# Optimization experiments

Measured on AMD Instinct MI355X. Metric: run time of the kernel, lower is better.

## Reference

```python
import jax, jax.numpy as jnp
import numpy as np

D_MODEL = 1024
N_HEADS = 16
D_HEAD = D_MODEL // N_HEADS
SCALE = D_HEAD ** -0.5


def setup_inputs() -> dict:
    key = jax.random.key(0)
    ks = jax.random.split(key, 9)
    s = 0.02
    x = jax.random.normal(ks[0], (2, 2048, D_MODEL), dtype=jnp.float32)
    Wq = jax.random.normal(ks[1], (D_MODEL, D_MODEL), dtype=jnp.float32) * s
    Wk = jax.random.normal(ks[2], (D_MODEL, D_MODEL), dtype=jnp.float32) * s
    Wv = jax.random.normal(ks[3], (D_MODEL, D_MODEL), dtype=jnp.float32) * s
    Wo = jax.random.normal(ks[4], (D_MODEL, D_MODEL), dtype=jnp.float32) * s
    bq = jax.random.normal(ks[5], (D_MODEL,), dtype=jnp.float32) * s
    bk = jax.random.normal(ks[6], (D_MODEL,), dtype=jnp.float32) * s
    bv = jax.random.normal(ks[7], (D_MODEL,), dtype=jnp.float32) * s
    bo = jax.random.normal(ks[8], (D_MODEL,), dtype=jnp.float32) * s
    return {"x": x, "Wq": Wq, "bq": bq, "Wk": Wk, "bk": bk,
            "Wv": Wv, "bv": bv, "Wo": Wo, "bo": bo}


def reference(x, Wq, bq, Wk, bk, Wv, bv, Wo, bo):
    B, S, _ = x.shape
    # torch nn.Linear: y = x @ W.T + b
    def proj(W, b):
        h = jnp.einsum('bsd,ed->bse', x, W) + b
        return h.reshape(B, S, N_HEADS, D_HEAD).transpose(0, 2, 1, 3)  # [B,H,S,Dh]
    Q = proj(Wq, bq)
    K = proj(Wk, bk)
    V = proj(Wv, bv)
    # chunked QK^T softmax over full K == full attention (no mask, dropout=0)
    scores = jnp.einsum('bhqd,bhkd->bhqk', Q, K) * SCALE  # [B,H,S,S]
    attn = jax.nn.softmax(scores, axis=-1)
    out = jnp.einsum('bhqk,bhkd->bhqd', attn, V)
    out = out.transpose(0, 2, 1, 3).reshape(B, S, D_MODEL)
    return jnp.einsum('bsd,ed->bse', out, Wo) + bo
```

## Files before the change

kernel.cpp:

```cpp
#include <hip/hip_runtime.h>
#include <cstdint>
#include <cstddef>


typedef unsigned short u16;
typedef unsigned int u32;
typedef __bf16 bf16x8 __attribute__((ext_vector_type(8)));
typedef float f32x4 __attribute__((ext_vector_type(4)));

#define GLOAD_LDS16(gp, lp)                                                            \
  __builtin_amdgcn_global_load_lds((const __attribute__((address_space(1))) void*)(gp),\
                                   (__attribute__((address_space(3))) void*)(lp),      \
                                   16, 0, 0)

__device__ __forceinline__ u16 f2bf(float f) {
  unsigned u = __builtin_bit_cast(unsigned, f);
  u = u + 0x7fffu + ((u >> 16) & 1u);
  return (u16)(u >> 16);
}

__device__ __forceinline__ u32 cvtpk(float a, float b) {
  u32 r;
  asm("v_cvt_pk_bf16_f32 %0, %1, %2" : "=v"(r) : "v"(a), "v"(b));
  return r;
}

#define QSCALE 0.1803368801111204f

__global__ void cvt_all(const float* __restrict__ x,
                        const float* __restrict__ wq, const float* __restrict__ wk,
                        const float* __restrict__ wv, const float* __restrict__ wo,
                        u16* __restrict__ xb, u16* __restrict__ wqb,
                        u16* __restrict__ wkb, u16* __restrict__ wvb,
                        u16* __restrict__ wob) {
  int bx = blockIdx.x;
  const float* s; u16* d; int off;
  if (bx < 2048)      { s = x;  d = xb;  off = bx; }
  else if (bx < 2560) { s = wq; d = wqb; off = bx - 2048; }
  else if (bx < 3072) { s = wk; d = wkb; off = bx - 2560; }
  else if (bx < 3584) { s = wv; d = wvb; off = bx - 3072; }
  else                { s = wo; d = wob; off = bx - 3584; }
  int i = off * 2048 + threadIdx.x * 8;
  float4 a = *(const float4*)(s + i);
  float4 b = *(const float4*)(s + i + 4);
  uint4 o;
  o.x = f2bf(a.x) | ((u32)f2bf(a.y) << 16);
  o.y = f2bf(a.z) | ((u32)f2bf(a.w) << 16);
  o.z = f2bf(b.x) | ((u32)f2bf(b.y) << 16);
  o.w = f2bf(b.z) | ((u32)f2bf(b.w) << 16);
  *(uint4*)(d + i) = o;
}

template <int MODE, int BM, int BN>
__global__ __launch_bounds__(256, MODE == 0 ? 3 : 4) void gemm_mfma(
    const u16* __restrict__ A,
    const u16* __restrict__ W0, const u16* __restrict__ W1, const u16* __restrict__ W2,
    const float* __restrict__ b0, const float* __restrict__ b1, const float* __restrict__ b2,
    u16* __restrict__ o0, u16* __restrict__ o1, u16* __restrict__ o2,
    float* __restrict__ oF)
{
  constexpr int MF = BM / 32;
  constexpr int NF = BN / 32;
  constexpr int AG = BM / 32;
  constexpr int BG = BN / 32;
  constexpr int KU = (MODE == 0) ? 1 : 2;

  __shared__ __align__(16) u16 As[KU][BM * 64];
  __shared__ __align__(16) u16 Bs[KU][BN * 64];

  const int tid = threadIdx.x;
  const int w = tid >> 6, l = tid & 63;
  const int lane = l & 15, quad = l >> 4;
  const int wm = w >> 1, wn = w & 1;

  const int idb = blockIdx.y * gridDim.x + blockIdx.x;
  const int xcd = idb & 7, j = idb >> 3;
  int m_idx, n_idx;
  if (MODE == 0) {
    m_idx = (xcd >> 1) * 8 + (j & 7);
    n_idx = (xcd & 1) * 12 + (j >> 3);
  } else {
    m_idx = (xcd >> 1) * 16 + (j & 15);
    n_idx = (xcd & 1) * 8 + (j >> 4);
  }
  const int m0 = m_idx * BM;
  const int n0g = n_idx * BN;

  const int src = (MODE == 0) ? (n0g >> 10) : 0;
  const u16* Wsel = (MODE == 0) ? (src == 0 ? W0 : (src == 1 ? W1 : W2)) : W0;
  const float* bsel = (MODE == 0) ? (src == 0 ? b0 : (src == 1 ? b1 : b2)) : b0;
  const int n_base = (MODE == 0) ? (n0g & 1023) : n0g;

  const int c8 = ((l & 7) ^ (l >> 3)) * 8;
  const int lrow = l >> 3;

  f32x4 acc[MF][NF] = {};

  for (int kt = 0; kt < 1024; kt += 64 * KU) {
    __syncthreads();
    #pragma unroll
    for (int ku = 0; ku < KU; ++ku) {
      const u16* Ag = A + (size_t)m0 * 1024 + kt + ku * 64;
      const u16* Bg = Wsel + (size_t)n_base * 1024 + kt + ku * 64;
      #pragma unroll
      for (int i = 0; i < AG; ++i) {
        int rr = w * (8 * AG) + i * 8;
        GLOAD_LDS16(Ag + (size_t)(rr + lrow) * 1024 + c8, As[ku] + rr * 64);
      }
      #pragma unroll
      for (int i = 0; i < BG; ++i) {
        int rr = w * (8 * BG) + i * 8;
        GLOAD_LDS16(Bg + (size_t)(rr + lrow) * 1024 + c8, Bs[ku] + rr * 64);
      }
    }
    __syncthreads();

    #pragma unroll
    for (int ku = 0; ku < KU; ++ku) {
      bf16x8 af[MF][2], bf[NF][2];
      #pragma unroll
      for (int mf = 0; mf < MF; ++mf)
        #pragma unroll
        for (int ks = 0; ks < 2; ++ks)
          af[mf][ks] = *(const bf16x8*)((const char*)As[ku] +
              (wm * (BM / 2) + mf * 16 + lane) * 128 + (((ks * 4 + quad) ^ (lane & 7)) * 16));
      #pragma unroll
      for (int nf = 0; nf < NF; ++nf)
        #pragma unroll
        for (int ks = 0; ks < 2; ++ks)
          bf[nf][ks] = *(const bf16x8*)((const char*)Bs[ku] +
              (wn * (BN / 2) + nf * 16 + lane) * 128 + (((ks * 4 + quad) ^ (lane & 7)) * 16));
      #pragma unroll
      for (int ks = 0; ks < 2; ++ks)
        #pragma unroll
        for (int mf = 0; mf < MF; ++mf)
          #pragma unroll
          for (int nf = 0; nf < NF; ++nf)
            acc[mf][nf] = __builtin_amdgcn_mfma_f32_16x16x32_bf16(
                af[mf][ks], bf[nf][ks], acc[mf][nf], 0, 0, 0);
    }
  }

  float bb[NF];
  #pragma unroll
  for (int nf = 0; nf < NF; ++nf)
    bb[nf] = bsel[n_base + wn * (BN / 2) + nf * 16 + lane];

  u16* osel = (MODE == 0) ? (src == 0 ? o0 : (src == 1 ? o1 : o2)) : o0;

  #pragma unroll
  for (int mf = 0; mf < MF; ++mf) {
    int mb = m0 + wm * (BM / 2) + mf * 16 + quad * 4;
    #pragma unroll
    for (int nf = 0; nf < NF; ++nf) {
      int n_l = wn * (BN / 2) + nf * 16 + lane;
      if (MODE == 0 && src != 1) {
        float sc = (src == 0) ? QSCALE : 1.0f;
        float v0 = (acc[mf][nf][0] + bb[nf]) * sc;
        float v1 = (acc[mf][nf][1] + bb[nf]) * sc;
        float v2 = (acc[mf][nf][2] + bb[nf]) * sc;
        float v3 = (acc[mf][nf][3] + bb[nf]) * sc;
        int bi = mb >> 11, s = mb & 2047;
        int n_in = n_base + n_l;
        int h = n_in >> 6, dh = n_in & 63;
        uint2 pk = make_uint2(cvtpk(v0, v1), cvtpk(v2, v3));
        *(uint2*)(osel + (((size_t)(bi * 16 + h) * 64 + dh) * 2048 + s)) = pk;
      } else {
        #pragma unroll
        for (int r = 0; r < 4; ++r) {
          float v = acc[mf][nf][r] + bb[nf];
          int m = mb + r;
          if (MODE == 0) {
            int bi = m >> 11, s = m & 2047;
            int n_in = n_base + n_l;
            int h = n_in >> 6, dh = n_in & 63;
            osel[(((size_t)(bi * 16 + h) * 2048 + s) << 6) + dh] = f2bf(v);
          } else {
            oF[(size_t)m * 1024 + n0g + n_l] = v;
          }
        }
      }
    }
  }
}

union SMemU {
  struct {
    u16 K[2][64 * 64];
    u16 V[2][64 * 64];
  } m;
  struct {
    float O[2][32 * 64];
    float L[2][32];
  } f;
};

__global__ __launch_bounds__(256, 4) void attn_mfma(
    const u16* __restrict__ Qg_, const u16* __restrict__ Kg_,
    const u16* __restrict__ VTg_, u16* __restrict__ Og)
{
  __shared__ __align__(16) SMemU sm;

  const int tid = threadIdx.x;
  const int w = tid >> 6, l = tid & 63;
  const int lane = l & 15, quad = l >> 4;
  const int g = w >> 1;
  const int kh = w & 1;

  const int idb = blockIdx.y * gridDim.x + blockIdx.x;
  const int lid = (idb & 7) * 128 + (idb >> 3);
  const int bh = lid >> 5;
  const int q0 = (lid & 31) * 64;

  const u16* QTg = Qg_ + (size_t)bh * 64 * 2048;
  const u16* Kg  = Kg_ + (size_t)bh * 2048 * 64;
  const u16* VTg = VTg_ + (size_t)bh * 64 * 2048;

  const int c8 = ((l & 7) ^ (l >> 3)) * 8;
  const int lrow = l >> 3;
  const int rr = w * 16;

  const int qcol = q0 + g * 32 + lane;
  bf16x8 bq[2][2];
  #pragma unroll
  for (int qf = 0; qf < 2; ++qf)
    #pragma unroll
    for (int ks = 0; ks < 2; ++ks) {
      bf16x8 v;
      #pragma unroll
      for (int j = 0; j < 8; ++j)
        v[j] = __builtin_bit_cast(__bf16,
            QTg[(size_t)(ks * 32 + quad * 8 + j) * 2048 + qcol + qf * 16]);
      bq[qf][ks] = v;
    }

  GLOAD_LDS16(Kg + (size_t)(rr + lrow) * 64 + c8, sm.m.K[0] + rr * 64);
  GLOAD_LDS16(Kg + (size_t)(rr + 8 + lrow) * 64 + c8, sm.m.K[0] + (rr + 8) * 64);
  GLOAD_LDS16(VTg + (size_t)(rr + lrow) * 2048 + c8, sm.m.V[0] + rr * 64);
  GLOAD_LDS16(VTg + (size_t)(rr + 8 + lrow) * 2048 + c8, sm.m.V[0] + (rr + 8) * 64);

  f32x4 oa[2][4] = {};
  float lsum[2] = {0.f, 0.f};

  for (int kt = 0; kt < 32; ++kt) {
    const int cur = kt & 1;
    asm volatile("s_waitcnt vmcnt(0)" ::: "memory");
    __builtin_amdgcn_s_barrier();
    asm volatile("" ::: "memory");

    if (kt < 31) {
      GLOAD_LDS16(Kg + (size_t)((kt + 1) * 64 + rr + lrow) * 64 + c8,
                  sm.m.K[cur ^ 1] + rr * 64);
      GLOAD_LDS16(Kg + (size_t)((kt + 1) * 64 + rr + 8 + lrow) * 64 + c8,
                  sm.m.K[cur ^ 1] + (rr + 8) * 64);
      GLOAD_LDS16(VTg + (size_t)(rr + lrow) * 2048 + (kt + 1) * 64 + c8,
                  sm.m.V[cur ^ 1] + rr * 64);
      GLOAD_LDS16(VTg + (size_t)(rr + 8 + lrow) * 2048 + (kt + 1) * 64 + c8,
                  sm.m.V[cur ^ 1] + (rr + 8) * 64);
    }

    f32x4 sa[2][2] = {};
    #pragma unroll
    for (int ks = 0; ks < 2; ++ks) {
      bf16x8 ak[2];
      #pragma unroll
      for (int kf = 0; kf < 2; ++kf)
        ak[kf] = *(const bf16x8*)((const char*)sm.m.K[cur] +
            (kh * 32 + kf * 16 + lane) * 128 + (((ks * 4 + quad) ^ (lane & 7)) * 16));
      #pragma unroll
      for (int kf = 0; kf < 2; ++kf)
        #pragma unroll
        for (int qf = 0; qf < 2; ++qf)
          sa[kf][qf] = __builtin_amdgcn_mfma_f32_16x16x32_bf16(
              ak[kf], bq[qf][ks], sa[kf][qf], 0, 0, 0);
    }

    bf16x8 ap[2];
    #pragma unroll
    for (int qf = 0; qf < 2; ++qf) {
      float x0 = __builtin_amdgcn_exp2f(sa[0][qf][0]);
      float x1 = __builtin_amdgcn_exp2f(sa[0][qf][1]);
      float x2 = __builtin_amdgcn_exp2f(sa[0][qf][2]);
      float x3 = __builtin_amdgcn_exp2f(sa[0][qf][3]);
      float y0 = __builtin_amdgcn_exp2f(sa[1][qf][0]);
      float y1 = __builtin_amdgcn_exp2f(sa[1][qf][1]);
      float y2 = __builtin_amdgcn_exp2f(sa[1][qf][2]);
      float y3 = __builtin_amdgcn_exp2f(sa[1][qf][3]);
      lsum[qf] += ((x0 + x1) + (x2 + x3)) + ((y0 + y1) + (y2 + y3));
      u32 X0 = cvtpk(x0, x1), X1 = cvtpk(x2, x3);
      u32 Y0 = cvtpk(y0, y1), Y1 = cvtpk(y2, y3);
      asm("v_permlane32_swap_b32 %0, %1" : "+v"(X0), "+v"(Y0));
      asm("v_permlane16_swap_b32 %0, %1" : "+v"(X0), "+v"(Y0));
      asm("v_permlane32_swap_b32 %0, %1" : "+v"(X1), "+v"(Y1));
      asm("v_permlane16_swap_b32 %0, %1" : "+v"(X1), "+v"(Y1));
      uint4 d4 = make_uint4(X0, X1, Y0, Y1);
      ap[qf] = __builtin_bit_cast(bf16x8, d4);
    }

    {
      bf16x8 bv[4];
      #pragma unroll
      for (int df = 0; df < 4; ++df)
        bv[df] = *(const bf16x8*)((const char*)sm.m.V[cur] +
            (df * 16 + lane) * 128 + (((kh * 4 + quad) ^ (lane & 7)) * 16));
      #pragma unroll
      for (int qf = 0; qf < 2; ++qf)
        #pragma unroll
        for (int df = 0; df < 4; ++df)
          oa[qf][df] = __builtin_amdgcn_mfma_f32_16x16x32_bf16(
              ap[qf], bv[df], oa[qf][df], 0, 0, 0);
    }
  }

  #pragma unroll
  for (int qf = 0; qf < 2; ++qf) {
    lsum[qf] += __shfl_xor(lsum[qf], 16);
    lsum[qf] += __shfl_xor(lsum[qf], 32);
  }

  __syncthreads();
  if (kh == 1) {
    #pragma unroll
    for (int qf = 0; qf < 2; ++qf)
      #pragma unroll
      for (int df = 0; df < 4; ++df)
        #pragma unroll
        for (int r = 0; r < 4; ++r)
          sm.f.O[g][(qf * 16 + quad * 4 + r) * 64 + df * 16 + lane] = oa[qf][df][r];
    if (l < 16) {
      sm.f.L[g][l] = lsum[0];
      sm.f.L[g][16 + l] = lsum[1];
    }
  }
  __syncthreads();
  if (kh == 0) {
    const int b = bh >> 4, hh = bh & 15;
    u16* Ob = Og + ((size_t)b * 2048 + q0 + g * 32) * 1024 + hh * 64;
    float ltot[2];
    #pragma unroll
    for (int qf = 0; qf < 2; ++qf)
      ltot[qf] = lsum[qf] + sm.f.L[g][qf * 16 + lane];
    #pragma unroll
    for (int qf = 0; qf < 2; ++qf)
      #pragma unroll
      for (int r = 0; r < 4; ++r) {
        float inv = 1.0f / __shfl(ltot[qf], quad * 4 + r, 16);
        int qrow = qf * 16 + quad * 4 + r;
        #pragma unroll
        for (int df = 0; df < 4; ++df) {
          float v = oa[qf][df][r] + sm.f.O[g][qrow * 64 + df * 16 + lane];
          Ob[(size_t)qrow * 1024 + df * 16 + lane] = f2bf(v * inv);
        }
      }
  }
}

extern "C" void kernel_launch(void* const* d_in, const int* in_sizes, int n_in,
                              void* d_out, int out_size, void* d_ws, size_t ws_size,
                              hipStream_t stream)
{
  (void)in_sizes; (void)n_in; (void)out_size; (void)ws_size;
  const float* x  = (const float*)d_in[0];
  const float* Wq = (const float*)d_in[1];
  const float* bq = (const float*)d_in[2];
  const float* Wk = (const float*)d_in[3];
  const float* bk = (const float*)d_in[4];
  const float* Wv = (const float*)d_in[5];
  const float* bv = (const float*)d_in[6];
  const float* Wo = (const float*)d_in[7];
  const float* bo = (const float*)d_in[8];
  float* y = (float*)d_out;

  const size_t NM = (size_t)4096 * 1024;
  u16* xb  = (u16*)d_ws;
  u16* wqb = xb + NM;
  u16* wkb = wqb + 1024 * 1024;
  u16* wvb = wkb + 1024 * 1024;
  u16* wob = wvb + 1024 * 1024;
  u16* Qb  = wob + 1024 * 1024;
  u16* Kb  = Qb + NM;
  u16* VTb = Kb + NM;
  u16* AOb = VTb + NM;

  cvt_all<<<4096, 256, 0, stream>>>(x, Wq, Wk, Wv, Wo, xb, wqb, wkb, wvb, wob);

  gemm_mfma<0, 128, 128><<<dim3(24, 32), 256, 0, stream>>>(
      xb, wqb, wkb, wvb, bq, bk, bv, Qb, Kb, VTb, nullptr);

  attn_mfma<<<dim3(32, 32), 256, 0, stream>>>(Qb, Kb, VTb, AOb);

  gemm_mfma<1, 64, 64><<<dim3(16, 64), 256, 0, stream>>>(
      AOb, wob, nullptr, nullptr, bo, nullptr, nullptr,
      nullptr, nullptr, nullptr, y);
}
```

Measured before the change: 178.7 us.

## Fuse all four kernels into one persistent kernel with grid-wide barriers

```diff
diff --git a/kernel.cpp b/kernel.cpp
--- a/kernel.cpp
+++ b/kernel.cpp
@@ -27,331 +27,361 @@
 
 #define QSCALE 0.1803368801111204f
 
-__global__ void cvt_all(const float* __restrict__ x,
-                        const float* __restrict__ wq, const float* __restrict__ wk,
-                        const float* __restrict__ wv, const float* __restrict__ wo,
-                        u16* __restrict__ xb, u16* __restrict__ wqb,
-                        u16* __restrict__ wkb, u16* __restrict__ wvb,
-                        u16* __restrict__ wob) {
-  int bx = blockIdx.x;
-  const float* s; u16* d; int off;
-  if (bx < 2048)      { s = x;  d = xb;  off = bx; }
-  else if (bx < 2560) { s = wq; d = wqb; off = bx - 2048; }
-  else if (bx < 3072) { s = wk; d = wkb; off = bx - 2560; }
-  else if (bx < 3584) { s = wv; d = wvb; off = bx - 3072; }
-  else                { s = wo; d = wob; off = bx - 3584; }
-  int i = off * 2048 + threadIdx.x * 8;
-  float4 a = *(const float4*)(s + i);
-  float4 b = *(const float4*)(s + i + 4);
-  uint4 o;
-  o.x = f2bf(a.x) | ((u32)f2bf(a.y) << 16);
-  o.y = f2bf(a.z) | ((u32)f2bf(a.w) << 16);
-  o.z = f2bf(b.x) | ((u32)f2bf(b.y) << 16);
-  o.w = f2bf(b.z) | ((u32)f2bf(b.w) << 16);
-  *(uint4*)(d + i) = o;
+union MegaSmem {
+  struct { u16 As[128 * 64]; u16 Bs[128 * 64]; } g0;
+  struct { u16 As[2][64 * 64]; u16 Bs[2][64 * 64]; } g1;
+  struct { u16 K[2][64 * 64]; u16 V[2][64 * 64]; } am;
+  struct { float O[2][32 * 64]; float L[2][32]; } af;
+};
+
+__device__ __forceinline__ void gbar(u32* c, u32 nblk) {
+  __syncthreads();
+  if (threadIdx.x == 0) {
+    __threadfence();
+    __hip_atomic_fetch_add(c, 1u, __ATOMIC_ACQ_REL, __HIP_MEMORY_SCOPE_AGENT);
+    while (__hip_atomic_load(c, __ATOMIC_RELAXED, __HIP_MEMORY_SCOPE_AGENT) < nblk)
+      __builtin_amdgcn_s_sleep(2);
+    __threadfence();
+  }
+  __syncthreads();
 }
 
-template <int MODE, int BM, int BN>
-__global__ __launch_bounds__(256, MODE == 0 ? 3 : 4) void gemm_mfma(
-    const u16* __restrict__ A,
-    const u16* __restrict__ W0, const u16* __restrict__ W1, const u16* __restrict__ W2,
-    const float* __restrict__ b0, const float* __restrict__ b1, const float* __restrict__ b2,
-    u16* __restrict__ o0, u16* __restrict__ o1, u16* __restrict__ o2,
-    float* __restrict__ oF)
+__global__ __launch_bounds__(256, 4) void mega(
+    const float* __restrict__ x,
+    const float* __restrict__ Wq, const float* __restrict__ bq,
+    const float* __restrict__ Wk, const float* __restrict__ bk,
+    const float* __restrict__ Wv, const float* __restrict__ bv,
+    const float* __restrict__ Wo, const float* __restrict__ bo,
+    u16* __restrict__ xb, u16* __restrict__ wqb, u16* __restrict__ wkb,
+    u16* __restrict__ wvb, u16* __restrict__ wob,
+    u16* __restrict__ Qb, u16* __restrict__ Kb, u16* __restrict__ VTb,
+    u16* __restrict__ AOb, float* __restrict__ y, u32* __restrict__ ctr)
 {
-  constexpr int MF = BM / 32;
-  constexpr int NF = BN / 32;
-  constexpr int AG = BM / 32;
-  constexpr int BG = BN / 32;
-  constexpr int KU = (MODE == 0) ? 1 : 2;
-
-  __shared__ __align__(16) u16 As[KU][BM * 64];
-  __shared__ __align__(16) u16 Bs[KU][BN * 64];
+  __shared__ __align__(16) MegaSmem sm;
 
   const int tid = threadIdx.x;
+  const int idb = blockIdx.x;
   const int w = tid >> 6, l = tid & 63;
   const int lane = l & 15, quad = l >> 4;
-  const int wm = w >> 1, wn = w & 1;
-
-  const int idb = blockIdx.y * gridDim.x + blockIdx.x;
-  const int xcd = idb & 7, j = idb >> 3;
-  int m_idx, n_idx;
-  if (MODE == 0) {
-    m_idx = (xcd >> 1) * 8 + (j & 7);
-    n_idx = (xcd & 1) * 12 + (j >> 3);
-  } else {
-    m_idx = (xcd >> 1) * 16 + (j & 15);
-    n_idx = (xcd & 1) * 8 + (j >> 4);
-  }
-  const int m0 = m_idx * BM;
-  const int n0g = n_idx * BN;
-
-  const int src = (MODE == 0) ? (n0g >> 10) : 0;
-  const u16* Wsel = (MODE == 0) ? (src == 0 ? W0 : (src == 1 ? W1 : W2)) : W0;
-  const float* bsel = (MODE == 0) ? (src == 0 ? b0 : (src == 1 ? b1 : b2)) : b0;
-  const int n_base = (MODE == 0) ? (n0g & 1023) : n0g;
-
   const int c8 = ((l & 7) ^ (l >> 3)) * 8;
   const int lrow = l >> 3;
 
-  f32x4 acc[MF][NF] = {};
-
-  for (int kt = 0; kt < 1024; kt += 64 * KU) {
-    __syncthreads();
-    #pragma unroll
-    for (int ku = 0; ku < KU; ++ku) {
-      const u16* Ag = A + (size_t)m0 * 1024 + kt + ku * 64;
-      const u16* Bg = Wsel + (size_t)n_base * 1024 + kt + ku * 64;
-      #pragma unroll
-      for (int i = 0; i < AG; ++i) {
-        int rr = w * (8 * AG) + i * 8;
-        GLOAD_LDS16(Ag + (size_t)(rr + lrow) * 1024 + c8, As[ku] + rr * 64);
-      }
-      #pragma unroll
-      for (int i = 0; i < BG; ++i) {
-        int rr = w * (8 * BG) + i * 8;
-        GLOAD_LDS16(Bg + (size_t)(rr + lrow) * 1024 + c8, Bs[ku] + rr * 64);
-      }
-    }
-    __syncthreads();
-
-    #pragma unroll
-    for (int ku = 0; ku < KU; ++ku) {
-      bf16x8 af[MF][2], bf[NF][2];
-      #pragma unroll
-      for (int mf = 0; mf < MF; ++mf)
-        #pragma unroll
-        for (int ks = 0; ks < 2; ++ks)
-          af[mf][ks] = *(const bf16x8*)((const char*)As[ku] +
-              (wm * (BM / 2) + mf * 16 + lane) * 128 + (((ks * 4 + quad) ^ (lane & 7)) * 16));
-      #pragma unroll
-      for (int nf = 0; nf < NF; ++nf)
-        #pragma unroll
-        for (int ks = 0; ks < 2; ++ks)
-          bf[nf][ks] = *(const bf16x8*)((const char*)Bs[ku] +
-              (wn * (BN / 2) + nf * 16 + lane) * 128 + (((ks * 4 + quad) ^ (lane & 7)) * 16));
-      #pragma unroll
-      for (int ks = 0; ks < 2; ++ks)
-        #pragma unroll
-        for (int mf = 0; mf < MF; ++mf)
-          #pragma unroll
-          for (int nf = 0; nf < NF; ++nf)
+  for (int u = idb; u < 4096; u += 1024) {
+    const float* s; u16* d; int off;
+    if (u < 2048)      { s = x;  d = xb;  off = u; }
+    else if (u < 2560) { s = Wq; d = wqb; off = u - 2048; }
+    else if (u < 3072) { s = Wk; d = wkb; off = u - 2560; }
+    else if (u < 3584) { s = Wv; d = wvb; off = u - 3072; }
+    else               { s = Wo; d = wob; off = u - 3584; }
+    int i = off * 2048 + tid * 8;
+    float4 a = *(const float4*)(s + i);
+    float4 b = *(const float4*)(s + i + 4);
+    uint4 o;
+    o.x = f2bf(a.x) | ((u32)f2bf(a.y) << 16);
+    o.y = f2bf(a.z) | ((u32)f2bf(a.w) << 16);
+    o.z = f2bf(b.x) | ((u32)f2bf(b.y) << 16);
+    o.w = f2bf(b.z) | ((u32)f2bf(b.w) << 16);
+    *(uint4*)(d + i) = o;
+  }
+  gbar(ctr + 0, 1024);
+
+  if (idb < 768) {
+    const int xcd = idb & 7, j = idb >> 3;
+    const int m_idx = (xcd >> 1) * 8 + (j & 7);
+    const int n_idx = (xcd & 1) * 12 + (j >> 3);
+    const int m0 = m_idx * 128;
+    const int n0g = n_idx * 128;
+    const int src = n0g >> 10;
+    const u16* Wsel = (src == 0) ? wqb : (src == 1 ? wkb : wvb);
+    const float* bsel = (src == 0) ? bq : (src == 1 ? bk : bv);
+    const int n_base = n0g & 1023;
+    const int wm = w >> 1, wn = w & 1;
+
+    f32x4 acc[4][4] = {};
+
+    for (int kt = 0; kt < 1024; kt += 64) {
+      __syncthreads();
+      const u16* Ag = xb + (size_t)m0 * 1024 + kt;
+      const u16* Bg = Wsel + (size_t)n_base * 1024 + kt;
+      #pragma unroll
+      for (int i = 0; i < 4; ++i) {
+        int rr = w * 32 + i * 8;
+        GLOAD_LDS16(Ag + (size_t)(rr + lrow) * 1024 + c8, sm.g0.As + rr * 64);
+        GLOAD_LDS16(Bg + (size_t)(rr + lrow) * 1024 + c8, sm.g0.Bs + rr * 64);
+      }
+      __syncthreads();
+
+      #pragma unroll
+      for (int ks = 0; ks < 2; ++ks) {
+        bf16x8 af[4], bf[4];
+        #pragma unroll
+        for (int mf = 0; mf < 4; ++mf)
+          af[mf] = *(const bf16x8*)((const char*)sm.g0.As +
+              (wm * 64 + mf * 16 + lane) * 128 + (((ks * 4 + quad) ^ (lane & 7)) * 16));
+        #pragma unroll
+        for (int nf = 0; nf < 4; ++nf)
+          bf[nf] = *(const bf16x8*)((const char*)sm.g0.Bs +
+              (wn * 64 + nf * 16 + lane) * 128 + (((ks * 4 + quad) ^ (lane & 7)) * 16));
+        #pragma unroll
+        for (int mf = 0; mf < 4; ++mf)
+          #pragma unroll
+          for (int nf = 0; nf < 4; ++nf)
             acc[mf][nf] = __builtin_amdgcn_mfma_f32_16x16x32_bf16(
-                af[mf][ks], bf[nf][ks], acc[mf][nf], 0, 0, 0);
-    }
-  }
-
-  float bb[NF];
-  #pragma unroll
-  for (int nf = 0; nf < NF; ++nf)
-    bb[nf] = bsel[n_base + wn * (BN / 2) + nf * 16 + lane];
-
-  u16* osel = (MODE == 0) ? (src == 0 ? o0 : (src == 1 ? o1 : o2)) : o0;
-
-  #pragma unroll
-  for (int mf = 0; mf < MF; ++mf) {
-    int mb = m0 + wm * (BM / 2) + mf * 16 + quad * 4;
-    #pragma unroll
-    for (int nf = 0; nf < NF; ++nf) {
-      int n_l = wn * (BN / 2) + nf * 16 + lane;
-      if (MODE == 0 && src != 1) {
-        float sc = (src == 0) ? QSCALE : 1.0f;
-        float v0 = (acc[mf][nf][0] + bb[nf]) * sc;
-        float v1 = (acc[mf][nf][1] + bb[nf]) * sc;
-        float v2 = (acc[mf][nf][2] + bb[nf]) * sc;
-        float v3 = (acc[mf][nf][3] + bb[nf]) * sc;
-        int bi = mb >> 11, s = mb & 2047;
-        int n_in = n_base + n_l;
-        int h = n_in >> 6, dh = n_in & 63;
-        uint2 pk = make_uint2(cvtpk(v0, v1), cvtpk(v2, v3));
-        *(uint2*)(osel + (((size_t)(bi * 16 + h) * 64 + dh) * 2048 + s)) = pk;
-      } else {
-        #pragma unroll
-        for (int r = 0; r < 4; ++r) {
-          float v = acc[mf][nf][r] + bb[nf];
-          int m = mb + r;
-          if (MODE == 0) {
+                af[mf], bf[nf], acc[mf][nf], 0, 0, 0);
+      }
+    }
+
+    float bb[4];
+    #pragma unroll
+    for (int nf = 0; nf < 4; ++nf) bb[nf] = bsel[n_base + wn * 64 + nf * 16 + lane];
+
+    u16* osel = (src == 0) ? Qb : (src == 1 ? Kb : VTb);
+
+    #pragma unroll
+    for (int mf = 0; mf < 4; ++mf) {
+      int mb = m0 + wm * 64 + mf * 16 + quad * 4;
+      #pragma unroll
+      for (int nf = 0; nf < 4; ++nf) {
+        int n_l = wn * 64 + nf * 16 + lane;
+        if (src != 1) {
+          float sc = (src == 0) ? QSCALE : 1.0f;
+          float v0 = (acc[mf][nf][0] + bb[nf]) * sc;
+          float v1 = (acc[mf][nf][1] + bb[nf]) * sc;
+          float v2 = (acc[mf][nf][2] + bb[nf]) * sc;
+          float v3 = (acc[mf][nf][3] + bb[nf]) * sc;
+          int bi = mb >> 11, s = mb & 2047;
+          int n_in = n_base + n_l;
+          int h = n_in >> 6, dh = n_in & 63;
+          uint2 pk = make_uint2(cvtpk(v0, v1), cvtpk(v2, v3));
+          *(uint2*)(osel + (((size_t)(bi * 16 + h) * 64 + dh) * 2048 + s)) = pk;
+        } else {
+          #pragma unroll
+          for (int r = 0; r < 4; ++r) {
+            float v = acc[mf][nf][r] + bb[nf];
+            int m = mb + r;
             int bi = m >> 11, s = m & 2047;
             int n_in = n_base + n_l;
             int h = n_in >> 6, dh = n_in & 63;
             osel[(((size_t)(bi * 16 + h) * 2048 + s) << 6) + dh] = f2bf(v);
-          } else {
-            oF[(size_t)m * 1024 + n0g + n_l] = v;
           }
         }
       }
     }
   }
-}
-
-union SMemU {
-  struct {
-    u16 K[2][64 * 64];
-    u16 V[2][64 * 64];
-  } m;
-  struct {
-    float O[2][32 * 64];
-    float L[2][32];
-  } f;
-};
-
-__global__ __launch_bounds__(256, 4) void attn_mfma(
-    const u16* __restrict__ Qg_, const u16* __restrict__ Kg_,
-    const u16* __restrict__ VTg_, u16* __restrict__ Og)
-{
-  __shared__ __align__(16) SMemU sm;
-
-  const int tid = threadIdx.x;
-  const int w = tid >> 6, l = tid & 63;
-  const int lane = l & 15, quad = l >> 4;
-  const int g = w >> 1;
-  const int kh = w & 1;
-
-  const int idb = blockIdx.y * gridDim.x + blockIdx.x;
-  const int lid = (idb & 7) * 128 + (idb >> 3);
-  const int bh = lid >> 5;
-  const int q0 = (lid & 31) * 64;
-
-  const u16* QTg = Qg_ + (size_t)bh * 64 * 2048;
-  const u16* Kg  = Kg_ + (size_t)bh * 2048 * 64;
-  const u16* VTg = VTg_ + (size_t)bh * 64 * 2048;
-
-  const int c8 = ((l & 7) ^ (l >> 3)) * 8;
-  const int lrow = l >> 3;
-  const int rr = w * 16;
-
-  const int qcol = q0 + g * 32 + lane;
-  bf16x8 bq[2][2];
-  #pragma unroll
-  for (int qf = 0; qf < 2; ++qf)
-    #pragma unroll
-    for (int ks = 0; ks < 2; ++ks) {
-      bf16x8 v;
-      #pragma unroll
-      for (int j = 0; j < 8; ++j)
-        v[j] = __builtin_bit_cast(__bf16,
-            QTg[(size_t)(ks * 32 + quad * 8 + j) * 2048 + qcol + qf * 16]);
-      bq[qf][ks] = v;
-    }
-
-  GLOAD_LDS16(Kg + (size_t)(rr + lrow) * 64 + c8, sm.m.K[0] + rr * 64);
-  GLOAD_LDS16(Kg + (size_t)(rr + 8 + lrow) * 64 + c8, sm.m.K[0] + (rr + 8) * 64);
-  GLOAD_LDS16(VTg + (size_t)(rr + lrow) * 2048 + c8, sm.m.V[0] + rr * 64);
-  GLOAD_LDS16(VTg + (size_t)(rr + 8 + lrow) * 2048 + c8, sm.m.V[0] + (rr + 8) * 64);
-
-  f32x4 oa[2][4] = {};
-  float lsum[2] = {0.f, 0.f};
-
-  for (int kt = 0; kt < 32; ++kt) {
-    const int cur = kt & 1;
-    asm volatile("s_waitcnt vmcnt(0)" ::: "memory");
-    __builtin_amdgcn_s_barrier();
-    asm volatile("" ::: "memory");
-
-    if (kt < 31) {
-      GLOAD_LDS16(Kg + (size_t)((kt + 1) * 64 + rr + lrow) * 64 + c8,
-                  sm.m.K[cur ^ 1] + rr * 64);
-      GLOAD_LDS16(Kg + (size_t)((kt + 1) * 64 + rr + 8 + lrow) * 64 + c8,
-                  sm.m.K[cur ^ 1] + (rr + 8) * 64);
-      GLOAD_LDS16(VTg + (size_t)(rr + lrow) * 2048 + (kt + 1) * 64 + c8,
-                  sm.m.V[cur ^ 1] + rr * 64);
-      GLOAD_LDS16(VTg + (size_t)(rr + 8 + lrow) * 2048 + (kt + 1) * 64 + c8,
-                  sm.m.V[cur ^ 1] + (rr + 8) * 64);
-    }
-
-    f32x4 sa[2][2] = {};
-    #pragma unroll
-    for (int ks = 0; ks < 2; ++ks) {
-      bf16x8 ak[2];
-      #pragma unroll
-      for (int kf = 0; kf < 2; ++kf)
-        ak[kf] = *(const bf16x8*)((const char*)sm.m.K[cur] +
-            (kh * 32 + kf * 16 + lane) * 128 + (((ks * 4 + quad) ^ (lane & 7)) * 16));
-      #pragma unroll
-      for (int kf = 0; kf < 2; ++kf)
+  gbar(ctr + 1, 1024);
+
+  {
+    const int g = w >> 1;
+    const int kh = w & 1;
+    const int lid = (idb & 7) * 128 + (idb >> 3);
+    const int bh = lid >> 5;
+    const int q0 = (lid & 31) * 64;
+
+    const u16* QTg = Qb + (size_t)bh * 64 * 2048;
+    const u16* Kg  = Kb + (size_t)bh * 2048 * 64;
+    const u16* VTg = VTb + (size_t)bh * 64 * 2048;
+
+    const int rr = w * 16;
+
+    const int qcol = q0 + g * 32 + lane;
+    bf16x8 bq_[2][2];
+    #pragma unroll
+    for (int qf = 0; qf < 2; ++qf)
+      #pragma unroll
+      for (int ks = 0; ks < 2; ++ks) {
+        bf16x8 v;
+        #pragma unroll
+        for (int jj = 0; jj < 8; ++jj)
+          v[jj] = __builtin_bit_cast(__bf16,
+              QTg[(size_t)(ks * 32 + quad * 8 + jj) * 2048 + qcol + qf * 16]);
+        bq_[qf][ks] = v;
+      }
+
+    GLOAD_LDS16(Kg + (size_t)(rr + lrow) * 64 + c8, sm.am.K[0] + rr * 64);
+    GLOAD_LDS16(Kg + (size_t)(rr + 8 + lrow) * 64 + c8, sm.am.K[0] + (rr + 8) * 64);
+    GLOAD_LDS16(VTg + (size_t)(rr + lrow) * 2048 + c8, sm.am.V[0] + rr * 64);
+    GLOAD_LDS16(VTg + (size_t)(rr + 8 + lrow) * 2048 + c8, sm.am.V[0] + (rr + 8) * 64);
+
+    f32x4 oa[2][4] = {};
+    float lsum[2] = {0.f, 0.f};
+
+    for (int kt = 0; kt < 32; ++kt) {
+      const int cur = kt & 1;
+      asm volatile("s_waitcnt vmcnt(0)" ::: "memory");
+      __builtin_amdgcn_s_barrier();
+      asm volatile("" ::: "memory");
+
+      if (kt < 31) {
+        GLOAD_LDS16(Kg + (size_t)((kt + 1) * 64 + rr + lrow) * 64 + c8,
+                    sm.am.K[cur ^ 1] + rr * 64);
+        GLOAD_LDS16(Kg + (size_t)((kt + 1) * 64 + rr + 8 + lrow) * 64 + c8,
+                    sm.am.K[cur ^ 1] + (rr + 8) * 64);
+        GLOAD_LDS16(VTg + (size_t)(rr + lrow) * 2048 + (kt + 1) * 64 + c8,
+                    sm.am.V[cur ^ 1] + rr * 64);
+        GLOAD_LDS16(VTg + (size_t)(rr + 8 + lrow) * 2048 + (kt + 1) * 64 + c8,
+                    sm.am.V[cur ^ 1] + (rr + 8) * 64);
+      }
+
+      f32x4 sa[2][2] = {};
+      #pragma unroll
+      for (int ks = 0; ks < 2; ++ks) {
+        bf16x8 ak[2];
+        #pragma unroll
+        for (int kf = 0; kf < 2; ++kf)
+          ak[kf] = *(const bf16x8*)((const char*)sm.am.K[cur] +
+              (kh * 32 + kf * 16 + lane) * 128 + (((ks * 4 + quad) ^ (lane & 7)) * 16));
+        #pragma unroll
+        for (int kf = 0; kf < 2; ++kf)
+          #pragma unroll
+          for (int qf = 0; qf < 2; ++qf)
+            sa[kf][qf] = __builtin_amdgcn_mfma_f32_16x16x32_bf16(
+                ak[kf], bq_[qf][ks], sa[kf][qf], 0, 0, 0);
+      }
+
+      bf16x8 ap[2];
+      #pragma unroll
+      for (int qf = 0; qf < 2; ++qf) {
+        float x0 = __builtin_amdgcn_exp2f(sa[0][qf][0]);
+        float x1 = __builtin_amdgcn_exp2f(sa[0][qf][1]);
+        float x2 = __builtin_amdgcn_exp2f(sa[0][qf][2]);
+        float x3 = __builtin_amdgcn_exp2f(sa[0][qf][3]);
+        float y0 = __builtin_amdgcn_exp2f(sa[1][qf][0]);
+        float y1 = __builtin_amdgcn_exp2f(sa[1][qf][1]);
+        float y2 = __builtin_amdgcn_exp2f(sa[1][qf][2]);
+        float y3 = __builtin_amdgcn_exp2f(sa[1][qf][3]);
+        lsum[qf] += ((x0 + x1) + (x2 + x3)) + ((y0 + y1) + (y2 + y3));
+        u32 X0 = cvtpk(x0, x1), X1 = cvtpk(x2, x3);
+        u32 Y0 = cvtpk(y0, y1), Y1 = cvtpk(y2, y3);
+        asm("v_permlane32_swap_b32 %0, %1" : "+v"(X0), "+v"(Y0));
+        asm("v_permlane16_swap_b32 %0, %1" : "+v"(X0), "+v"(Y0));
+        asm("v_permlane32_swap_b32 %0, %1" : "+v"(X1), "+v"(Y1));
+        asm("v_permlane16_swap_b32 %0, %1" : "+v"(X1), "+v"(Y1));
+        uint4 d4 = make_uint4(X0, X1, Y0, Y1);
+        ap[qf] = __builtin_bit_cast(bf16x8, d4);
+      }
+
+      {
+        bf16x8 bv_[4];
+        #pragma unroll
+        for (int df = 0; df < 4; ++df)
+          bv_[df] = *(const bf16x8*)((const char*)sm.am.V[cur] +
+              (df * 16 + lane) * 128 + (((kh * 4 + quad) ^ (lane & 7)) * 16));
         #pragma unroll
         for (int qf = 0; qf < 2; ++qf)
-          sa[kf][qf] = __builtin_amdgcn_mfma_f32_16x16x32_bf16(
-              ak[kf], bq[qf][ks], sa[kf][qf], 0, 0, 0);
-    }
-
-    bf16x8 ap[2];
+          #pragma unroll
+          for (int df = 0; df < 4; ++df)
+            oa[qf][df] = __builtin_amdgcn_mfma_f32_16x16x32_bf16(
+                ap[qf], bv_[df], oa[qf][df], 0, 0, 0);
+      }
+    }
+
     #pragma unroll
     for (int qf = 0; qf < 2; ++qf) {
-      float x0 = __builtin_amdgcn_exp2f(sa[0][qf][0]);
-      float x1 = __builtin_amdgcn_exp2f(sa[0][qf][1]);
-      float x2 = __builtin_amdgcn_exp2f(sa[0][qf][2]);
-      float x3 = __builtin_amdgcn_exp2f(sa[0][qf][3]);
-      float y0 = __builtin_amdgcn_exp2f(sa[1][qf][0]);
-      float y1 = __builtin_amdgcn_exp2f(sa[1][qf][1]);
-      float y2 = __builtin_amdgcn_exp2f(sa[1][qf][2]);
-      float y3 = __builtin_amdgcn_exp2f(sa[1][qf][3]);
-      lsum[qf] += ((x0 + x1) + (x2 + x3)) + ((y0 + y1) + (y2 + y3));
-      u32 X0 = cvtpk(x0, x1), X1 = cvtpk(x2, x3);
-      u32 Y0 = cvtpk(y0, y1), Y1 = cvtpk(y2, y3);
-      asm("v_permlane32_swap_b32 %0, %1" : "+v"(X0), "+v"(Y0));
-      asm("v_permlane16_swap_b32 %0, %1" : "+v"(X0), "+v"(Y0));
-      asm("v_permlane32_swap_b32 %0, %1" : "+v"(X1), "+v"(Y1));
-      asm("v_permlane16_swap_b32 %0, %1" : "+v"(X1), "+v"(Y1));
-      uint4 d4 = make_uint4(X0, X1, Y0, Y1);
-      ap[qf] = __builtin_bit_cast(bf16x8, d4);
-    }
-
-    {
-      bf16x8 bv[4];
-      #pragma unroll
-      for (int df = 0; df < 4; ++df)
-        bv[df] = *(const bf16x8*)((const char*)sm.m.V[cur] +
-            (df * 16 + lane) * 128 + (((kh * 4 + quad) ^ (lane & 7)) * 16));
+      lsum[qf] += __shfl_xor(lsum[qf], 16);
+      lsum[qf] += __shfl_xor(lsum[qf], 32);
+    }
+
+    __syncthreads();
+    if (kh == 1) {
       #pragma unroll
       for (int qf = 0; qf < 2; ++qf)
         #pragma unroll
         for (int df = 0; df < 4; ++df)
-          oa[qf][df] = __builtin_amdgcn_mfma_f32_16x16x32_bf16(
-              ap[qf], bv[df], oa[qf][df], 0, 0, 0);
+          #pragma unroll
+          for (int r = 0; r < 4; ++r)
+            sm.af.O[g][(qf * 16 + quad * 4 + r) * 64 + df * 16 + lane] = oa[qf][df][r];
+      if (l < 16) {
+        sm.af.L[g][l] = lsum[0];
+        sm.af.L[g][16 + l] = lsum[1];
+      }
+    }
+    __syncthreads();
+    if (kh == 0) {
+      const int b = bh >> 4, hh = bh & 15;
+      u16* Ob = AOb + ((size_t)b * 2048 + q0 + g * 32) * 1024 + hh * 64;
+      float ltot[2];
+      #pragma unroll
+      for (int qf = 0; qf < 2; ++qf)
+        ltot[qf] = lsum[qf] + sm.af.L[g][qf * 16 + lane];
+      #pragma unroll
+      for (int qf = 0; qf < 2; ++qf)
+        #pragma unroll
+        for (int r = 0; r < 4; ++r) {
+          float inv = 1.0f / __shfl(ltot[qf], quad * 4 + r, 16);
+          int qrow = qf * 16 + quad * 4 + r;
+          #pragma unroll
+          for (int df = 0; df < 4; ++df) {
+            float v = oa[qf][df][r] + sm.af.O[g][qrow * 64 + df * 16 + lane];
+            Ob[(size_t)qrow * 1024 + df * 16 + lane] = f2bf(v * inv);
+          }
+        }
     }
   }
-
-  #pragma unroll
-  for (int qf = 0; qf < 2; ++qf) {
-    lsum[qf] += __shfl_xor(lsum[qf], 16);
-    lsum[qf] += __shfl_xor(lsum[qf], 32);
-  }
-
-  __syncthreads();
-  if (kh == 1) {
-    #pragma unroll
-    for (int qf = 0; qf < 2; ++qf)
-      #pragma unroll
-      for (int df = 0; df < 4; ++df)
+  gbar(ctr + 2, 1024);
+
+  {
+    const int xcd = idb & 7, j = idb >> 3;
+    const int m_idx = (xcd >> 1) * 16 + (j & 15);
+    const int n_idx = (xcd & 1) * 8 + (j >> 4);
+    const int m0 = m_idx * 64;
+    const int n0g = n_idx * 64;
+    const int wm = w >> 1, wn = w & 1;
+
+    f32x4 acc[2][2] = {};
+
+    for (int kt = 0; kt < 1024; kt += 128) {
+      __syncthreads();
+      #pragma unroll
+      for (int ku = 0; ku < 2; ++ku) {
+        const u16* Ag = AOb + (size_t)m0 * 1024 + kt + ku * 64;
+        const u16* Bg = wob + (size_t)n0g * 1024 + kt + ku * 64;
+        {
+          int rr = w * 16;
+          GLOAD_LDS16(Ag + (size_t)(rr + lrow) * 1024 + c8, sm.g1.As[ku] + rr * 64);
+          GLOAD_LDS16(Ag + (size_t)(rr + 8 + lrow) * 1024 + c8, sm.g1.As[ku] + (rr + 8) * 64);
+          GLOAD_LDS16(Bg + (size_t)(rr + lrow) * 1024 + c8, sm.g1.Bs[ku] + rr * 64);
+          GLOAD_LDS16(Bg + (size_t)(rr + 8 + lrow) * 1024 + c8, sm.g1.Bs[ku] + (rr + 8) * 64);
+        }
+      }
+      __syncthreads();
+
+      #pragma unroll
+      for (int ku = 0; ku < 2; ++ku)
+        #pragma unroll
+        for (int ks = 0; ks < 2; ++ks) {
+          bf16x8 af[2], bf[2];
+          #pragma unroll
+          for (int mf = 0; mf < 2; ++mf)
+            af[mf] = *(const bf16x8*)((const char*)sm.g1.As[ku] +
+                (wm * 32 + mf * 16 + lane) * 128 + (((ks * 4 + quad) ^ (lane & 7)) * 16));
+          #pragma unroll
+          for (int nf = 0; nf < 2; ++nf)
+            bf[nf] = *(const bf16x8*)((const char*)sm.g1.Bs[ku] +
+                (wn * 32 + nf * 16 + lane) * 128 + (((ks * 4 + quad) ^ (lane & 7)) * 16));
+          #pragma unroll
+          for (int mf = 0; mf < 2; ++mf)
+            #pragma unroll
+            for (int nf = 0; nf < 2; ++nf)
+              acc[mf][nf] = __builtin_amdgcn_mfma_f32_16x16x32_bf16(
+                  af[mf], bf[nf], acc[mf][nf], 0, 0, 0);
+        }
+    }
+
+    float bb[2];
+    #pragma unroll
+    for (int nf = 0; nf < 2; ++nf) bb[nf] = bo[n0g + wn * 32 + nf * 16 + lane];
+
+    #pragma unroll
+    for (int mf = 0; mf < 2; ++mf) {
+      int mb = m0 + wm * 32 + mf * 16 + quad * 4;
+      #pragma unroll
+      for (int nf = 0; nf < 2; ++nf) {
+        int n_l = wn * 32 + nf * 16 + lane;
         #pragma unroll
         for (int r = 0; r < 4; ++r)
-          sm.f.O[g][(qf * 16 + quad * 4 + r) * 64 + df * 16 + lane] = oa[qf][df][r];
-    if (l < 16) {
-      sm.f.L[g][l] = lsum[0];
-      sm.f.L[g][16 + l] = lsum[1];
-    }
-  }
-  __syncthreads();
-  if (kh == 0) {
-    const int b = bh >> 4, hh = bh & 15;
-    u16* Ob = Og + ((size_t)b * 2048 + q0 + g * 32) * 1024 + hh * 64;
-    float ltot[2];
-    #pragma unroll
-    for (int qf = 0; qf < 2; ++qf)
-      ltot[qf] = lsum[qf] + sm.f.L[g][qf * 16 + lane];
-    #pragma unroll
-    for (int qf = 0; qf < 2; ++qf)
-      #pragma unroll
-      for (int r = 0; r < 4; ++r) {
-        float inv = 1.0f / __shfl(ltot[qf], quad * 4 + r, 16);
-        int qrow = qf * 16 + quad * 4 + r;
-        #pragma unroll
-        for (int df = 0; df < 4; ++df) {
-          float v = oa[qf][df][r] + sm.f.O[g][qrow * 64 + df * 16 + lane];
-          Ob[(size_t)qrow * 1024 + df * 16 + lane] = f2bf(v * inv);
-        }
-      }
+          y[(size_t)(mb + r) * 1024 + n0g + n_l] = acc[mf][nf][r] + bb[nf];
+      }
+    }
   }
 }
 
@@ -381,15 +411,11 @@
   u16* Kb  = Qb + NM;
   u16* VTb = Kb + NM;
   u16* AOb = VTb + NM;
-
-  cvt_all<<<4096, 256, 0, stream>>>(x, Wq, Wk, Wv, Wo, xb, wqb, wkb, wvb, wob);
-
-  gemm_mfma<0, 128, 128><<<dim3(24, 32), 256, 0, stream>>>(
-      xb, wqb, wkb, wvb, bq, bk, bv, Qb, Kb, VTb, nullptr);
-
-  attn_mfma<<<dim3(32, 32), 256, 0, stream>>>(Qb, Kb, VTb, AOb);
-
-  gemm_mfma<1, 64, 64><<<dim3(16, 64), 256, 0, stream>>>(
-      AOb, wob, nullptr, nullptr, bo, nullptr, nullptr,
-      nullptr, nullptr, nullptr, y);
+  u32* ctr = (u32*)(AOb + NM);
+
+  hipMemsetAsync(ctr, 0, 16, stream);
+
+  mega<<<1024, 256, 0, stream>>>(x, Wq, bq, Wk, bk, Wv, bv, Wo, bo,
+                                 xb, wqb, wkb, wvb, wob,
+                                 Qb, Kb, VTb, AOb, y, ctr);
 }
```

New measurement: 546.2 us. 3.06x slower.
